# Kernel tuning notes

Hardware: AMD Instinct MI355X
Metric: run time of the kernel (lower is better)

The kernel has to match this reference:

```python
import jax, jax.numpy as jnp
import numpy as np

B, S, E = 4096, 200, 32

def setup_inputs() -> dict:
    key = jax.random.key(0)
    ks = jax.random.split(key, 8)
    scale = 1.0 / np.sqrt(E)
    return {
        "all_memory": jax.random.normal(ks[0], (B, S, E), jnp.float32),
        "last_memory": jax.random.normal(ks[1], (B, E), jnp.float32),
        "average_memory": jax.random.normal(ks[2], (B, E), jnp.float32),
        "mask": jnp.zeros((B, S), dtype=bool),
        "W1": jax.random.normal(ks[3], (E, E), jnp.float32) * scale,
        "b1": jnp.zeros((E,), jnp.float32),
        "W2": jax.random.normal(ks[4], (E, E), jnp.float32) * scale,
        "b2": jnp.zeros((E,), jnp.float32),
        "W3": jax.random.normal(ks[5], (E, E), jnp.float32) * scale,
        "b3": jnp.zeros((E,), jnp.float32),
        "W4": jax.random.normal(ks[6], (E, 1), jnp.float32) * scale,
    }


def reference(all_memory, last_memory, average_memory, mask, W1, b1, W2, b2, W3, b3, W4):
    # all_memory: [B,S,E]; last/average_memory: [B,E]
    # NOTE: source has `if mask is None: masked_fill_`, so with a provided
    # (non-None) mask the masking branch is dead code -> mask unused.
    proj = (jnp.einsum('bse,ef->bsf', all_memory, W1) + b1
            + (last_memory @ W2 + b2)[:, None, :]
            + (average_memory @ W3 + b3)[:, None, :])  # [B,S,E]
    scores = jax.nn.sigmoid(proj) @ W4  # [B,S,1]
    out = jnp.sum(scores * all_memory, axis=1)  # [B,E]
    return out
```

## Files before the change

### kernel.cpp

```cpp
#include <hip/hip_runtime.h>

#define B_N 4096
#define S_N 200
#define E_N 32

typedef float f32x4 __attribute__((ext_vector_type(4)));
typedef short s16x8 __attribute__((ext_vector_type(8)));

static __device__ __forceinline__ unsigned short f2bf(float f) {
    unsigned u = __builtin_bit_cast(unsigned, f);
    u += 0x7fffu + ((u >> 16) & 1u);
    return (unsigned short)(u >> 16);
}

__global__ __launch_bounds__(256, 4) void attn_pool_kernel(
    const float* __restrict__ am,
    const float* __restrict__ lastm,
    const float* __restrict__ avgm,
    const float* __restrict__ W1,
    const float* __restrict__ b1,
    const float* __restrict__ W2,
    const float* __restrict__ b2,
    const float* __restrict__ W3,
    const float* __restrict__ b3,
    const float* __restrict__ W4,
    float* __restrict__ out)
{
    const int tid  = threadIdx.x;
    const int l    = tid & 63;
    const int wave = tid >> 6;
    const int b    = blockIdx.x * 4 + wave;

    const int lm = l & 15;
    const int lg = l >> 4;
    const int fi = l & 31;

    float lastv = lastm[b * E_N + fi];
    float avgv  = avgm [b * E_N + fi];
    float base_f = b1[fi] + b2[fi] + b3[fi];
#pragma unroll
    for (int e = 0; e < E_N; ++e) {
        float le = __shfl(lastv, e);
        float ae = __shfl(avgv,  e);
        base_f += le * W2[e * E_N + fi] + ae * W3[e * E_N + fi];
    }
    float baseA = __shfl(base_f, lm);
    float baseB = __shfl(base_f, 16 + lm);
    float w4A = W4[lm];
    float w4B = W4[16 + lm];

    s16x8 bfA, bfB;
#pragma unroll
    for (int i = 0; i < 8; ++i) {
        int k = 8 * lg + i;
        bfA[i] = (short)f2bf(W1[k * E_N + lm]);
        bfB[i] = (short)f2bf(W1[k * E_N + 16 + lm]);
    }

    float acc[8];
#pragma unroll
    for (int i = 0; i < 8; ++i) acc[i] = 0.0f;

    const int e0 = 8 * lg;

    for (int t = 0; t < 13; ++t) {
        const int r = t * 16 + lm;
        float amf[8];
        if (r < S_N) {
            const f32x4* p = (const f32x4*)(am + ((size_t)b * S_N + r) * E_N + e0);
            f32x4 v0 = p[0];
            f32x4 v1 = p[1];
#pragma unroll
            for (int i = 0; i < 4; ++i) { amf[i] = v0[i]; amf[4 + i] = v1[i]; }
        } else {
#pragma unroll
            for (int i = 0; i < 8; ++i) amf[i] = 0.0f;
        }

        s16x8 af;
#pragma unroll
        for (int i = 0; i < 8; ++i) af[i] = (short)f2bf(amf[i]);

        f32x4 z = {0.0f, 0.0f, 0.0f, 0.0f};
        f32x4 d0 = __builtin_amdgcn_mfma_f32_16x16x32_bf16(af, bfA, z, 0, 0, 0);
        f32x4 d1 = __builtin_amdgcn_mfma_f32_16x16x32_bf16(af, bfB, z, 0, 0, 0);

        float sc[4];
#pragma unroll
        for (int j = 0; j < 4; ++j) {
            float pA = d0[j] + baseA;
            float pB = d1[j] + baseB;
            float sA = 1.0f / (1.0f + __expf(-pA));
            float sB = 1.0f / (1.0f + __expf(-pB));
            sc[j] = sA * w4A + sB * w4B;
        }
#pragma unroll
        for (int j = 0; j < 4; ++j) {
            sc[j] += __shfl_xor(sc[j], 1);
            sc[j] += __shfl_xor(sc[j], 2);
            sc[j] += __shfl_xor(sc[j], 4);
            sc[j] += __shfl_xor(sc[j], 8);
        }
        const int src = (lm >> 2) << 4;
        float t0 = __shfl(sc[0], src);
        float t1 = __shfl(sc[1], src);
        float t2 = __shfl(sc[2], src);
        float t3 = __shfl(sc[3], src);
        const int jj = lm & 3;
        float score = (jj == 0) ? t0 : (jj == 1) ? t1 : (jj == 2) ? t2 : t3;

#pragma unroll
        for (int i = 0; i < 8; ++i) acc[i] += score * amf[i];
    }

#pragma unroll
    for (int i = 0; i < 8; ++i) {
        acc[i] += __shfl_xor(acc[i], 1);
        acc[i] += __shfl_xor(acc[i], 2);
        acc[i] += __shfl_xor(acc[i], 4);
        acc[i] += __shfl_xor(acc[i], 8);
    }
    if (lm == 0) {
        f32x4 o0, o1;
#pragma unroll
        for (int i = 0; i < 4; ++i) { o0[i] = acc[i]; o1[i] = acc[4 + i]; }
        f32x4* po = (f32x4*)(out + (size_t)b * E_N + e0);
        po[0] = o0;
        po[1] = o1;
    }
}

extern "C" void kernel_launch(void* const* d_in, const int* in_sizes, int n_in,
                              void* d_out, int out_size, void* d_ws, size_t ws_size,
                              hipStream_t stream) {
    const float* am    = (const float*)d_in[0];
    const float* lastm = (const float*)d_in[1];
    const float* avgm  = (const float*)d_in[2];
    const float* W1 = (const float*)d_in[4];
    const float* b1 = (const float*)d_in[5];
    const float* W2 = (const float*)d_in[6];
    const float* b2 = (const float*)d_in[7];
    const float* W3 = (const float*)d_in[8];
    const float* b3 = (const float*)d_in[9];
    const float* W4 = (const float*)d_in[10];
    float* out = (float*)d_out;

    dim3 grid(B_N / 4);
    dim3 block(256);
    hipLaunchKernelGGL(attn_pool_kernel, grid, block, 0, stream,
                       am, lastm, avgm, W1, b1, W2, b2, W3, b3, W4, out);
}
```

Before: 177.7 us.

## Transpose MFMA operands to cut score reductions and prefetch next tile

The MFMA operand order is swapped so that each lane's output column corresponds to one sequence row, with the feature dimension spread across lane groups. The per-row score then needs only two xor-shuffles instead of sixteen shuffles plus a select. The kernel also software-prefetches the next 16-row tile into registers, uses hardware packed bf16 conversion in place of manual rounding, and uses a fast reciprocal for the sigmoid. These changes raise register use and slightly reduce sigmoid precision.

```diff
diff --git a/kernel.cpp b/kernel.cpp
--- a/kernel.cpp
+++ b/kernel.cpp
@@ -1,4 +1,5 @@
 #include <hip/hip_runtime.h>
+#include <hip/hip_bf16.h>
 
 #define B_N 4096
 #define S_N 200
@@ -6,12 +7,6 @@
 
 typedef float f32x4 __attribute__((ext_vector_type(4)));
 typedef short s16x8 __attribute__((ext_vector_type(8)));
-
-static __device__ __forceinline__ unsigned short f2bf(float f) {
-    unsigned u = __builtin_bit_cast(unsigned, f);
-    u += 0x7fffu + ((u >> 16) & 1u);
-    return (unsigned short)(u >> 16);
-}
 
 __global__ __launch_bounds__(256, 4) void attn_pool_kernel(
     const float* __restrict__ am,
@@ -35,8 +30,8 @@
     const int lg = l >> 4;
     const int fi = l & 31;
 
-    float lastv = lastm[b * E_N + fi];
-    float avgv  = avgm [b * E_N + fi];
+    float lastv  = lastm[b * E_N + fi];
+    float avgv   = avgm [b * E_N + fi];
     float base_f = b1[fi] + b2[fi] + b3[fi];
 #pragma unroll
     for (int e = 0; e < E_N; ++e) {
@@ -44,73 +39,81 @@
         float ae = __shfl(avgv,  e);
         base_f += le * W2[e * E_N + fi] + ae * W3[e * E_N + fi];
     }
-    float baseA = __shfl(base_f, lm);
-    float baseB = __shfl(base_f, 16 + lm);
-    float w4A = W4[lm];
-    float w4B = W4[16 + lm];
+    float baseA[4], baseB[4], w4A[4], w4B[4];
+#pragma unroll
+    for (int j = 0; j < 4; ++j) {
+        baseA[j] = __shfl(base_f, 4 * lg + j);
+        baseB[j] = __shfl(base_f, 16 + 4 * lg + j);
+        w4A[j]   = W4[4 * lg + j];
+        w4B[j]   = W4[16 + 4 * lg + j];
+    }
 
-    s16x8 bfA, bfB;
+    s16x8 w1A, w1B;
 #pragma unroll
-    for (int i = 0; i < 8; ++i) {
-        int k = 8 * lg + i;
-        bfA[i] = (short)f2bf(W1[k * E_N + lm]);
-        bfB[i] = (short)f2bf(W1[k * E_N + 16 + lm]);
+    for (int i = 0; i < 8; i += 2) {
+        int e = 8 * lg + i;
+        float2 a0 = {W1[e * E_N + lm],        W1[(e + 1) * E_N + lm]};
+        float2 a1 = {W1[e * E_N + 16 + lm],   W1[(e + 1) * E_N + 16 + lm]};
+        ((__hip_bfloat162*)&w1A)[i >> 1] = __float22bfloat162_rn(a0);
+        ((__hip_bfloat162*)&w1B)[i >> 1] = __float22bfloat162_rn(a1);
     }
+
+    const int e0 = 8 * lg;
+    const float* rowbase = am + (size_t)b * S_N * E_N + e0;
 
     float acc[8];
 #pragma unroll
     for (int i = 0; i < 8; ++i) acc[i] = 0.0f;
 
-    const int e0 = 8 * lg;
+    float amf[8], nxt[8];
+    {
+        const f32x4* p = (const f32x4*)(rowbase + (size_t)lm * E_N);
+        f32x4 v0 = p[0], v1 = p[1];
+#pragma unroll
+        for (int i = 0; i < 4; ++i) { amf[i] = v0[i]; amf[4 + i] = v1[i]; }
+    }
 
+#pragma unroll 2
     for (int t = 0; t < 13; ++t) {
-        const int r = t * 16 + lm;
-        float amf[8];
-        if (r < S_N) {
-            const f32x4* p = (const f32x4*)(am + ((size_t)b * S_N + r) * E_N + e0);
-            f32x4 v0 = p[0];
-            f32x4 v1 = p[1];
+        if (t < 12) {
+            const int r = (t + 1) * 16 + lm;
+            if (r < S_N) {
+                const f32x4* p = (const f32x4*)(rowbase + (size_t)r * E_N);
+                f32x4 v0 = p[0], v1 = p[1];
 #pragma unroll
-            for (int i = 0; i < 4; ++i) { amf[i] = v0[i]; amf[4 + i] = v1[i]; }
-        } else {
+                for (int i = 0; i < 4; ++i) { nxt[i] = v0[i]; nxt[4 + i] = v1[i]; }
+            } else {
 #pragma unroll
-            for (int i = 0; i < 8; ++i) amf[i] = 0.0f;
+                for (int i = 0; i < 8; ++i) nxt[i] = 0.0f;
+            }
         }
 
         s16x8 af;
 #pragma unroll
-        for (int i = 0; i < 8; ++i) af[i] = (short)f2bf(amf[i]);
+        for (int i = 0; i < 8; i += 2) {
+            float2 a = {amf[i], amf[i + 1]};
+            ((__hip_bfloat162*)&af)[i >> 1] = __float22bfloat162_rn(a);
+        }
 
         f32x4 z = {0.0f, 0.0f, 0.0f, 0.0f};
-        f32x4 d0 = __builtin_amdgcn_mfma_f32_16x16x32_bf16(af, bfA, z, 0, 0, 0);
-        f32x4 d1 = __builtin_amdgcn_mfma_f32_16x16x32_bf16(af, bfB, z, 0, 0, 0);
+        f32x4 d0 = __builtin_amdgcn_mfma_f32_16x16x32_bf16(w1A, af, z, 0, 0, 0);
+        f32x4 d1 = __builtin_amdgcn_mfma_f32_16x16x32_bf16(w1B, af, z, 0, 0, 0);
 
-        float sc[4];
+        float s = 0.0f;
 #pragma unroll
         for (int j = 0; j < 4; ++j) {
-            float pA = d0[j] + baseA;
-            float pB = d1[j] + baseB;
-            float sA = 1.0f / (1.0f + __expf(-pA));
-            float sB = 1.0f / (1.0f + __expf(-pB));
-            sc[j] = sA * w4A + sB * w4B;
+            float pA = d0[j] + baseA[j];
+            float pB = d1[j] + baseB[j];
+            s += w4A[j] * __builtin_amdgcn_rcpf(1.0f + __expf(-pA));
+            s += w4B[j] * __builtin_amdgcn_rcpf(1.0f + __expf(-pB));
         }
-#pragma unroll
-        for (int j = 0; j < 4; ++j) {
-            sc[j] += __shfl_xor(sc[j], 1);
-            sc[j] += __shfl_xor(sc[j], 2);
-            sc[j] += __shfl_xor(sc[j], 4);
-            sc[j] += __shfl_xor(sc[j], 8);
-        }
-        const int src = (lm >> 2) << 4;
-        float t0 = __shfl(sc[0], src);
-        float t1 = __shfl(sc[1], src);
-        float t2 = __shfl(sc[2], src);
-        float t3 = __shfl(sc[3], src);
-        const int jj = lm & 3;
-        float score = (jj == 0) ? t0 : (jj == 1) ? t1 : (jj == 2) ? t2 : t3;
+        s += __shfl_xor(s, 16);
+        s += __shfl_xor(s, 32);
 
 #pragma unroll
-        for (int i = 0; i < 8; ++i) acc[i] += score * amf[i];
+        for (int i = 0; i < 8; ++i) acc[i] += s * amf[i];
+#pragma unroll
+        for (int i = 0; i < 8; ++i) amf[i] = nxt[i];
     }
 
 #pragma unroll
```

Measured after the change: 211.0 us. 1.19x slower.
